# Optimization experiments

Hardware: AMD Instinct MI355X
Metric: run time of the kernel (lower is better)

Reference implementation:

```python
import jax, jax.numpy as jnp
import numpy as np

C, K, H = 256, 64, 1024


def squash(t):
    # t: [C, H]; norm = sum of squares over last dim (matches torch code)
    norm = jnp.sum(t * t, axis=-1, keepdims=True)  # [C, 1]
    scale = norm / (1.0 + norm)
    return scale * t / jnp.sqrt(norm)


def setup_inputs() -> dict:
    key = jax.random.key(0)
    k1, k2 = jax.random.split(key)
    encoder_output = jax.random.normal(k1, (C, K, H), dtype=jnp.float32)
    # nn.Linear weight [out, in]; scaled init for numerical sanity
    W = jax.random.normal(k2, (H, H), dtype=jnp.float32) * (1.0 / np.sqrt(H))
    return {"encoder_output": encoder_output, "W": W, "iter_routing": 3}


def reference(encoder_output, W, iter_routing):
    # encoder_output: [C, K, H], W: [H, H] (l_1 weight, no bias)
    # The linear projection is loop-invariant in the original; hoist it.
    x_hat = jnp.einsum('ckh,dh->ckd', encoder_output, W)  # [C, K, H]
    b = jnp.zeros(encoder_output.shape[:2], dtype=encoder_output.dtype)  # [C, K]
    c = None
    for _ in range(iter_routing):
        d = jax.nn.softmax(b, axis=-1)                       # [C, K]
        c_hat = jnp.sum(x_hat * d[..., None], axis=1)        # [C, H]
        c = squash(c_hat)                                    # [C, H]
        b = b + jnp.einsum('ckh,ch->ck', x_hat, c)           # [C, K]
    return c
```

## Files before the change

### kernel.cpp

```cpp
#include <hip/hip_runtime.h>


using f32x4  = __attribute__((ext_vector_type(4))) float;
using f32x2  = __attribute__((ext_vector_type(2))) float;
using bf16x8 = __attribute__((ext_vector_type(8))) __bf16;
using bf16x4 = __attribute__((ext_vector_type(4))) __bf16;

struct BfPair { __bf16 hi, lo; };
__device__ inline BfPair split_bf16(float x) {
    BfPair p;
    p.hi = (__bf16)x;
    p.lo = (__bf16)(x - (float)p.hi);
    return p;
}

template <int MODE>
__global__ __launch_bounds__(1024, 4) void routing_kernel(
    const float* __restrict__ enc, const float* __restrict__ y0,
    const float* __restrict__ y1, float* __restrict__ bglob,
    __bf16* __restrict__ s_hi, __bf16* __restrict__ s_lo)
{
    __shared__ float spart[16][1024];
    __shared__ float u_s[1024];
    __shared__ float b_s[64], d_s[64], red_s[16], scale_s;

    const int t = threadIdx.x, lane = t & 63, w = t >> 6;
    const int c = blockIdx.x;
    const float* E = enc + (size_t)c * 65536;

    float yv = 0.f, sv = 0.f;
    if (MODE > 0) {
        const size_t o = (size_t)c * 1024 + t;
        yv = y0[o] + y1[o];
        sv = (float)s_hi[o] + (float)s_lo[o];
    }

    f32x4 er[4][4];
    #pragma unroll
    for (int r = 0; r < 4; ++r) {
        const float* ek = E + (size_t)(w * 4 + r) * 1024 + lane * 8;
        er[r][0] = *(const f32x4*)(ek);
        er[r][1] = *(const f32x4*)(ek + 4);
        er[r][2] = *(const f32x4*)(ek + 512);
        er[r][3] = *(const f32x4*)(ek + 516);
    }
    #pragma unroll
    for (int r = 0; r < 4; ++r)
        #pragma unroll
        for (int q = 0; q < 4; ++q)
            asm volatile("" : "+v"(er[r][q]));

    if (MODE > 0) {
        u_s[t] = yv;
        float p = yv * sv;
        #pragma unroll
        for (int off = 32; off; off >>= 1) p += __shfl_xor(p, off, 64);
        if (lane == 0) red_s[w] = p;
        __syncthreads();
        if (t == 0) {
            float n = 0.f;
            #pragma unroll
            for (int i = 0; i < 16; ++i) n += red_s[i];
            scale_s = n / ((1.f + n) * sqrtf(n) + 1e-30f);
        }
        __syncthreads();
        const float scale = scale_s;
        f32x4 uf[4];
        uf[0] = *(const f32x4*)&u_s[lane * 8];
        uf[1] = *(const f32x4*)&u_s[lane * 8 + 4];
        uf[2] = *(const f32x4*)&u_s[512 + lane * 8];
        uf[3] = *(const f32x4*)&u_s[512 + lane * 8 + 4];
        #pragma unroll
        for (int r = 0; r < 4; ++r) {
            float sum = 0.f;
            #pragma unroll
            for (int q = 0; q < 4; ++q)
                #pragma unroll
                for (int j = 0; j < 4; ++j)
                    sum += er[r][q][j] * uf[q][j];
            #pragma unroll
            for (int off = 32; off; off >>= 1) sum += __shfl_xor(sum, off, 64);
            if (lane == 0) {
                const int k = w * 4 + r;
                const float bv =
                    (MODE == 2 ? bglob[c * 64 + k] : 0.f) + scale * sum;
                bglob[c * 64 + k] = bv;
                b_s[k] = bv;
            }
        }
    }
    __syncthreads();

    if (MODE == 0) {
        if (t < 64) d_s[t] = 1.f / 64.f;
    } else if (t < 64) {
        float bv = b_s[t], m = bv;
        #pragma unroll
        for (int off = 32; off; off >>= 1) m = fmaxf(m, __shfl_xor(m, off, 64));
        const float e = expf(bv - m);
        float sm = e;
        #pragma unroll
        for (int off = 32; off; off >>= 1) sm += __shfl_xor(sm, off, 64);
        d_s[t] = e / sm;
    }
    __syncthreads();

    #pragma unroll
    for (int q = 0; q < 4; ++q) {
        f32x4 p = {};
        #pragma unroll
        for (int r = 0; r < 4; ++r) {
            const float dk = d_s[w * 4 + r];
            #pragma unroll
            for (int j = 0; j < 4; ++j) p[j] += dk * er[r][q][j];
        }
        const int h = (q >> 1) * 512 + lane * 8 + (q & 1) * 4;
        *(f32x4*)&spart[w][h] = p;
    }
    __syncthreads();

    {
        float a = 0.f;
        #pragma unroll
        for (int wv = 0; wv < 16; ++wv) a += spart[wv][t];
        const BfPair p = split_bf16(a);
        s_hi[(size_t)c * 1024 + t] = p.hi;
        s_lo[(size_t)c * 1024 + t] = p.lo;
    }
}

struct QSmem {
    __bf16 a_hi[64 * 64];
    __bf16 a_lo[64 * 64];
    __bf16 b_hi[64 * 64];
    __bf16 b_lo[64 * 64];
};

__device__ __forceinline__ int swz128(int row, int colbyte) {
    return row * 128 + (colbyte ^ ((row & 7) << 4));
}

__global__ __launch_bounds__(256) void gemm_q_kernel(
    const __bf16* __restrict__ Wt_hi, const __bf16* __restrict__ Wt_lo,
    __bf16* __restrict__ Q_hi, __bf16* __restrict__ Q_lo)
{
    __shared__ QSmem sm;
    const int qb = blockIdx.x;
    const int ti = qb >> 4, tj = qb & 15;
    const int t = threadIdx.x;
    const int lane = t & 63, w = t >> 6;
    const int wr = w >> 1, wc = w & 1;
    const int sr  = t >> 2;
    const int scb = (t & 3) * 16;
    const size_t ga = (size_t)(ti * 64 + sr) * 1024 + scb / 2;
    const size_t gb = (size_t)(tj * 64 + sr) * 1024 + scb / 2;

    f32x4 acc[2][2] = {};
    for (int k0 = 0; k0 < 1024; k0 += 64) {
        if (k0) __syncthreads();
        #pragma unroll
        for (int h = 0; h < 2; ++h) {
            const int cb = scb + h * 64;
            const size_t gao = ga + h * 32 + k0;
            const size_t gbo = gb + h * 32 + k0;
            *(bf16x8*)((char*)sm.a_hi + swz128(sr, cb)) = *(const bf16x8*)(Wt_hi + gao);
            *(bf16x8*)((char*)sm.a_lo + swz128(sr, cb)) = *(const bf16x8*)(Wt_lo + gao);
            *(bf16x8*)((char*)sm.b_hi + swz128(sr, cb)) = *(const bf16x8*)(Wt_hi + gbo);
            *(bf16x8*)((char*)sm.b_lo + swz128(sr, cb)) = *(const bf16x8*)(Wt_lo + gbo);
        }
        __syncthreads();
        #pragma unroll
        for (int kk = 0; kk < 2; ++kk) {
            const int cb = kk * 64 + (lane >> 4) * 16;
            bf16x8 ah[2], al[2], bh[2], bl[2];
            #pragma unroll
            for (int mi = 0; mi < 2; ++mi) {
                const int m = wr * 32 + mi * 16 + (lane & 15);
                ah[mi] = *(const bf16x8*)((char*)sm.a_hi + swz128(m, cb));
                al[mi] = *(const bf16x8*)((char*)sm.a_lo + swz128(m, cb));
            }
            #pragma unroll
            for (int ni = 0; ni < 2; ++ni) {
                const int n = wc * 32 + ni * 16 + (lane & 15);
                bh[ni] = *(const bf16x8*)((char*)sm.b_hi + swz128(n, cb));
                bl[ni] = *(const bf16x8*)((char*)sm.b_lo + swz128(n, cb));
            }
            #pragma unroll
            for (int mi = 0; mi < 2; ++mi)
                #pragma unroll
                for (int ni = 0; ni < 2; ++ni) {
                    f32x4 a = acc[mi][ni];
                    a = __builtin_amdgcn_mfma_f32_16x16x32_bf16(ah[mi], bh[ni], a, 0, 0, 0);
                    a = __builtin_amdgcn_mfma_f32_16x16x32_bf16(ah[mi], bl[ni], a, 0, 0, 0);
                    a = __builtin_amdgcn_mfma_f32_16x16x32_bf16(al[mi], bh[ni], a, 0, 0, 0);
                    acc[mi][ni] = a;
                }
        }
    }
    const int rr = (lane >> 4) * 4, colb = lane & 15;
    #pragma unroll
    for (int mi = 0; mi < 2; ++mi)
        #pragma unroll
        for (int ni = 0; ni < 2; ++ni)
            #pragma unroll
            for (int r = 0; r < 4; ++r) {
                const BfPair p = split_bf16(acc[mi][ni][r]);
                const size_t idx =
                    (size_t)(ti * 64 + wr * 32 + mi * 16 + rr + r) * 1024 +
                    tj * 64 + wc * 32 + ni * 16 + colb;
                Q_hi[idx] = p.hi;
                Q_lo[idx] = p.lo;
            }
}

template <int CONV>
__global__ __launch_bounds__(256) void gemm_split_kernel(
    const __bf16* __restrict__ Ah, const __bf16* __restrict__ Al,
    const __bf16* __restrict__ Bh, const __bf16* __restrict__ Bl,
    float* __restrict__ C0, float* __restrict__ C1,
    const float* __restrict__ Wsrc, __bf16* __restrict__ Wd_hi,
    __bf16* __restrict__ Wd_lo)
{
    if (CONV && blockIdx.x >= 512) {
        const int b = blockIdx.x - 512;
        const size_t base = (size_t)b * 4096 + (threadIdx.x << 2);
        #pragma unroll
        for (int q = 0; q < 4; ++q) {
            const size_t idx = base + (size_t)q * 1024;
            const f32x4 v = *(const f32x4*)(Wsrc + idx);
            bf16x4 hv, lv;
            #pragma unroll
            for (int j = 0; j < 4; ++j) {
                const BfPair p = split_bf16(v[j]);
                hv[j] = p.hi;
                lv[j] = p.lo;
            }
            *(bf16x4*)(Wd_hi + idx) = hv;
            *(bf16x4*)(Wd_lo + idx) = lv;
        }
        return;
    }

    const int w = threadIdx.x >> 6;
    const int gw = blockIdx.x * 4 + w;
    const int task = gw >> 1;
    const int kh   = gw & 1;
    const int mt   = task >> 6;
    const int nt   = task & 63;
    const int lane = threadIdx.x & 63;
    const int kq   = (lane >> 4) * 8 + kh * 512;
    const size_t aoff = (size_t)(mt * 16 + (lane & 15)) * 1024 + kq;
    const size_t boff = (size_t)(nt * 16 + (lane & 15)) * 1024 + kq;

    f32x4 hh = {}, hl = {}, lh = {};
    #pragma unroll 4
    for (int k0 = 0; k0 < 512; k0 += 32) {
        bf16x8 ah = *(const bf16x8*)(Ah + aoff + k0);
        bf16x8 al = *(const bf16x8*)(Al + aoff + k0);
        bf16x8 bh = *(const bf16x8*)(Bh + boff + k0);
        bf16x8 bl = *(const bf16x8*)(Bl + boff + k0);
        hh = __builtin_amdgcn_mfma_f32_16x16x32_bf16(ah, bh, hh, 0, 0, 0);
        hl = __builtin_amdgcn_mfma_f32_16x16x32_bf16(ah, bl, hl, 0, 0, 0);
        lh = __builtin_amdgcn_mfma_f32_16x16x32_bf16(al, bh, lh, 0, 0, 0);
    }
    f32x4 acc = hh + hl + lh;
    float* Cc = kh ? C1 : C0;
    const int rr = (lane >> 4) * 4, colb = lane & 15;
    #pragma unroll
    for (int r = 0; r < 4; ++r)
        Cc[(size_t)(mt * 16 + rr + r) * 1024 + nt * 16 + colb] = acc[r];
}

__global__ __launch_bounds__(256) void squash_out_kernel(
    const float* __restrict__ chat0, const float* __restrict__ chat1,
    float* __restrict__ outp)
{
    __shared__ float wsum[4];
    const int c = blockIdx.x, t = threadIdx.x;
    const int lane = t & 63, w = t >> 6;
    const size_t o = (size_t)c * 1024 + t * 4;
    f32x4 v = *(const f32x4*)(chat0 + o) + *(const f32x4*)(chat1 + o);
    float ss = v[0]*v[0] + v[1]*v[1] + v[2]*v[2] + v[3]*v[3];
    #pragma unroll
    for (int off = 32; off; off >>= 1) ss += __shfl_xor(ss, off, 64);
    if (lane == 0) wsum[w] = ss;
    __syncthreads();
    const float norm = wsum[0] + wsum[1] + wsum[2] + wsum[3];
    const float scale = norm / ((1.f + norm) * sqrtf(norm) + 1e-30f);
    *(f32x4*)(outp + o) = v * scale;
}

__global__ __launch_bounds__(256) void convert_wt_kernel(
    const float* __restrict__ W, __bf16* __restrict__ Wt_hi,
    __bf16* __restrict__ Wt_lo)
{
    __shared__ float tile[64][65];
    const int bx = blockIdx.x, by = blockIdx.y;
    const int tx = threadIdx.x & 63, ty = threadIdx.x >> 6;
    for (int i = ty; i < 64; i += 4)
        tile[i][tx] = W[(size_t)(by * 64 + i) * 1024 + bx * 64 + tx];
    __syncthreads();
    for (int i = ty; i < 64; i += 4) {
        const size_t idx = (size_t)(bx * 64 + i) * 1024 + by * 64 + tx;
        const BfPair p = split_bf16(tile[tx][i]);
        Wt_hi[idx] = p.hi;
        Wt_lo[idx] = p.lo;
    }
}

__global__ __launch_bounds__(512) void fallback_kernel(
    const float* __restrict__ enc, const float* __restrict__ W,
    float* __restrict__ outp)
{
    __shared__ float u_s[1024], s_s[1024], c_s[1024], chat_s[1024];
    __shared__ float b_s[64], d_s[64], red_s[8];
    const int t = threadIdx.x, lane = t & 63, w = t >> 6;
    const float* erow = enc + (size_t)blockIdx.x * 65536;

    if (t < 64) b_s[t] = 0.f;
    __syncthreads();

    for (int it = 0; it < 3; ++it) {
        if (it > 0) {
            f32x4 uf[4];
            #pragma unroll
            for (int q = 0; q < 2; ++q) {
                uf[2*q]   = *(const f32x4*)&u_s[q*512 + lane*8];
                uf[2*q+1] = *(const f32x4*)&u_s[q*512 + lane*8 + 4];
            }
            for (int r = 0; r < 8; ++r) {
                const int k = w * 8 + r;
                const float* ek = erow + (size_t)k * 1024;
                float sum = 0.f;
                #pragma unroll
                for (int q = 0; q < 2; ++q) {
                    f32x4 e0 = *(const f32x4*)(ek + q*512 + lane*8);
                    f32x4 e1 = *(const f32x4*)(ek + q*512 + lane*8 + 4);
                    #pragma unroll
                    for (int j = 0; j < 4; ++j) {
                        sum += e0[j] * uf[2*q][j];
                        sum += e1[j] * uf[2*q+1][j];
                    }
                }
                #pragma unroll
                for (int off = 32; off; off >>= 1) sum += __shfl_xor(sum, off, 64);
                if (lane == 0) b_s[k] += sum;
            }
            __syncthreads();
        }
        if (t < 64) {
            float bv = b_s[t], m = bv;
            #pragma unroll
            for (int off = 32; off; off >>= 1) m = fmaxf(m, __shfl_xor(m, off, 64));
            float e = expf(bv - m), sm = e;
            #pragma unroll
            for (int off = 32; off; off >>= 1) sm += __shfl_xor(sm, off, 64);
            d_s[t] = e / sm;
        }
        __syncthreads();
        {
            const int h0 = t * 2;
            float a0 = 0.f, a1 = 0.f;
            for (int k = 0; k < 64; ++k) {
                f32x2 ev = *(const f32x2*)(erow + (size_t)k * 1024 + h0);
                a0 += d_s[k] * ev[0]; a1 += d_s[k] * ev[1];
            }
            s_s[h0] = a0; s_s[h0+1] = a1;
        }
        __syncthreads();
        {
            f32x4 sf[4];
            #pragma unroll
            for (int q = 0; q < 2; ++q) {
                sf[2*q]   = *(const f32x4*)&s_s[q*512 + lane*8];
                sf[2*q+1] = *(const f32x4*)&s_s[q*512 + lane*8 + 4];
            }
            for (int r = 0; r < 128; ++r) {
                const int d = w * 128 + r;
                const float* wr = W + (size_t)d * 1024;
                float sum = 0.f;
                #pragma unroll
                for (int q = 0; q < 2; ++q) {
                    f32x4 w0 = *(const f32x4*)(wr + q*512 + lane*8);
                    f32x4 w1 = *(const f32x4*)(wr + q*512 + lane*8 + 4);
                    #pragma unroll
                    for (int j = 0; j < 4; ++j) {
                        sum += w0[j] * sf[2*q][j];
                        sum += w1[j] * sf[2*q+1][j];
                    }
                }
                #pragma unroll
                for (int off = 32; off; off >>= 1) sum += __shfl_xor(sum, off, 64);
                if (lane == 0) chat_s[d] = sum;
            }
        }
        __syncthreads();
        {
            const int h0 = t * 2;
            float v0 = chat_s[h0], v1 = chat_s[h0+1];
            float ss = v0*v0 + v1*v1;
            #pragma unroll
            for (int off = 32; off; off >>= 1) ss += __shfl_xor(ss, off, 64);
            if (lane == 0) red_s[w] = ss;
            __syncthreads();
            float norm = 0.f;
            #pragma unroll
            for (int i = 0; i < 8; ++i) norm += red_s[i];
            const float scale = norm / ((1.f + norm) * sqrtf(norm) + 1e-30f);
            c_s[h0] = v0 * scale; c_s[h0+1] = v1 * scale;
        }
        __syncthreads();
        if (it < 2) {
            const int h0 = t * 2;
            float uu0 = 0.f, uu1 = 0.f;
            for (int d = 0; d < 1024; ++d) {
                f32x2 wv = *(const f32x2*)(W + (size_t)d * 1024 + h0);
                uu0 += c_s[d] * wv[0]; uu1 += c_s[d] * wv[1];
            }
            u_s[h0] = uu0; u_s[h0+1] = uu1;
        } else {
            const int h0 = t * 2;
            f32x2 ov; ov[0] = c_s[h0]; ov[1] = c_s[h0+1];
            *(f32x2*)(outp + (size_t)blockIdx.x * 1024 + h0) = ov;
        }
        __syncthreads();
    }
}

extern "C" void kernel_launch(void* const* d_in, const int* in_sizes, int n_in,
                              void* d_out, int out_size, void* d_ws, size_t ws_size,
                              hipStream_t stream)
{
    const float* enc = (const float*)d_in[0];
    const float* W   = (const float*)d_in[1];
    float* outp = (float*)d_out;
    (void)in_sizes; (void)n_in; (void)out_size;

    char* ws = (char*)d_ws;
    float*  b     = (float*) (ws + 0x000000);
    __bf16* s_hi  = (__bf16*)(ws + 0x080000);
    __bf16* s_lo  = (__bf16*)(ws + 0x100000);
    float*  y0    = (float*) (ws + 0x180000);
    float*  y1    = (float*) (ws + 0x280000);
    __bf16* Wx_hi = (__bf16*)(ws + 0x380000);
    __bf16* Wx_lo = (__bf16*)(ws + 0x580000);
    __bf16* Q_hi  = (__bf16*)(ws + 0x780000);
    __bf16* Q_lo  = (__bf16*)(ws + 0x980000);

    if (ws_size < 0xB80000) {
        fallback_kernel<<<256, 512, 0, stream>>>(enc, W, outp);
        return;
    }

    convert_wt_kernel<<<dim3(16, 16), 256, 0, stream>>>(W, Wx_hi, Wx_lo);

    gemm_q_kernel<<<256, 256, 0, stream>>>(Wx_hi, Wx_lo, Q_hi, Q_lo);

    routing_kernel<0><<<256, 1024, 0, stream>>>(enc, y0, y1, b, s_hi, s_lo);

    gemm_split_kernel<1><<<768, 256, 0, stream>>>(
        s_hi, s_lo, Q_hi, Q_lo, y0, y1, W, Wx_hi, Wx_lo);

    routing_kernel<1><<<256, 1024, 0, stream>>>(enc, y0, y1, b, s_hi, s_lo);

    gemm_split_kernel<0><<<512, 256, 0, stream>>>(
        s_hi, s_lo, Q_hi, Q_lo, y0, y1, nullptr, nullptr, nullptr);

    routing_kernel<2><<<256, 1024, 0, stream>>>(enc, y0, y1, b, s_hi, s_lo);

    gemm_split_kernel<0><<<512, 256, 0, stream>>>(
        s_hi, s_lo, Wx_hi, Wx_lo, y0, y1, nullptr, nullptr, nullptr);

    squash_out_kernel<<<256, 256, 0, stream>>>(y0, y1, outp);
}
```

Before: 199.2 us.

## Tile split-bf16 GEMMs through swizzled LDS and fuse W conversion into routing

```diff
diff --git a/kernel.cpp b/kernel.cpp
--- a/kernel.cpp
+++ b/kernel.cpp
@@ -14,18 +14,19 @@
     return p;
 }
 
+struct RoutSM {
+    float spart[16][1024];
+    float u_s[1024];
+    float b_s[64], d_s[64], red_s[16], scale_s;
+};
+
 template <int MODE>
-__global__ __launch_bounds__(1024, 4) void routing_kernel(
-    const float* __restrict__ enc, const float* __restrict__ y0,
+__device__ __forceinline__ void routing_body(
+    int c, const float* __restrict__ enc, const float* __restrict__ y0,
     const float* __restrict__ y1, float* __restrict__ bglob,
-    __bf16* __restrict__ s_hi, __bf16* __restrict__ s_lo)
-{
-    __shared__ float spart[16][1024];
-    __shared__ float u_s[1024];
-    __shared__ float b_s[64], d_s[64], red_s[16], scale_s;
-
+    __bf16* __restrict__ s_hi, __bf16* __restrict__ s_lo, RoutSM* sm)
+{
     const int t = threadIdx.x, lane = t & 63, w = t >> 6;
-    const int c = blockIdx.x;
     const float* E = enc + (size_t)c * 65536;
 
     float yv = 0.f, sv = 0.f;
@@ -51,25 +52,25 @@
             asm volatile("" : "+v"(er[r][q]));
 
     if (MODE > 0) {
-        u_s[t] = yv;
+        sm->u_s[t] = yv;
         float p = yv * sv;
         #pragma unroll
         for (int off = 32; off; off >>= 1) p += __shfl_xor(p, off, 64);
-        if (lane == 0) red_s[w] = p;
+        if (lane == 0) sm->red_s[w] = p;
         __syncthreads();
         if (t == 0) {
             float n = 0.f;
             #pragma unroll
-            for (int i = 0; i < 16; ++i) n += red_s[i];
-            scale_s = n / ((1.f + n) * sqrtf(n) + 1e-30f);
-        }
-        __syncthreads();
-        const float scale = scale_s;
+            for (int i = 0; i < 16; ++i) n += sm->red_s[i];
+            sm->scale_s = n / ((1.f + n) * sqrtf(n) + 1e-30f);
+        }
+        __syncthreads();
+        const float scale = sm->scale_s;
         f32x4 uf[4];
-        uf[0] = *(const f32x4*)&u_s[lane * 8];
-        uf[1] = *(const f32x4*)&u_s[lane * 8 + 4];
-        uf[2] = *(const f32x4*)&u_s[512 + lane * 8];
-        uf[3] = *(const f32x4*)&u_s[512 + lane * 8 + 4];
+        uf[0] = *(const f32x4*)&sm->u_s[lane * 8];
+        uf[1] = *(const f32x4*)&sm->u_s[lane * 8 + 4];
+        uf[2] = *(const f32x4*)&sm->u_s[512 + lane * 8];
+        uf[3] = *(const f32x4*)&sm->u_s[512 + lane * 8 + 4];
         #pragma unroll
         for (int r = 0; r < 4; ++r) {
             float sum = 0.f;
@@ -85,23 +86,23 @@
                 const float bv =
                     (MODE == 2 ? bglob[c * 64 + k] : 0.f) + scale * sum;
                 bglob[c * 64 + k] = bv;
-                b_s[k] = bv;
+                sm->b_s[k] = bv;
             }
         }
     }
     __syncthreads();
 
     if (MODE == 0) {
-        if (t < 64) d_s[t] = 1.f / 64.f;
+        if (t < 64) sm->d_s[t] = 1.f / 64.f;
     } else if (t < 64) {
-        float bv = b_s[t], m = bv;
+        float bv = sm->b_s[t], m = bv;
         #pragma unroll
         for (int off = 32; off; off >>= 1) m = fmaxf(m, __shfl_xor(m, off, 64));
         const float e = expf(bv - m);
-        float sm = e;
-        #pragma unroll
-        for (int off = 32; off; off >>= 1) sm += __shfl_xor(sm, off, 64);
-        d_s[t] = e / sm;
+        float smm = e;
+        #pragma unroll
+        for (int off = 32; off; off >>= 1) smm += __shfl_xor(smm, off, 64);
+        sm->d_s[t] = e / smm;
     }
     __syncthreads();
 
@@ -110,23 +111,57 @@
         f32x4 p = {};
         #pragma unroll
         for (int r = 0; r < 4; ++r) {
-            const float dk = d_s[w * 4 + r];
+            const float dk = sm->d_s[w * 4 + r];
             #pragma unroll
             for (int j = 0; j < 4; ++j) p[j] += dk * er[r][q][j];
         }
         const int h = (q >> 1) * 512 + lane * 8 + (q & 1) * 4;
-        *(f32x4*)&spart[w][h] = p;
+        *(f32x4*)&sm->spart[w][h] = p;
     }
     __syncthreads();
 
     {
         float a = 0.f;
         #pragma unroll
-        for (int wv = 0; wv < 16; ++wv) a += spart[wv][t];
+        for (int wv = 0; wv < 16; ++wv) a += sm->spart[wv][t];
         const BfPair p = split_bf16(a);
         s_hi[(size_t)c * 1024 + t] = p.hi;
         s_lo[(size_t)c * 1024 + t] = p.lo;
     }
+}
+
+template <int MODE, int WITH_CONV>
+__global__ __launch_bounds__(1024, 4) void routing_kernel(
+    const float* __restrict__ enc, const float* __restrict__ y0,
+    const float* __restrict__ y1, float* __restrict__ bglob,
+    __bf16* __restrict__ s_hi, __bf16* __restrict__ s_lo,
+    const float* __restrict__ W, __bf16* __restrict__ Wt_hi,
+    __bf16* __restrict__ Wt_lo)
+{
+    __shared__ union {
+        RoutSM r;
+        float tile[64][65];
+    } sm;
+
+    int c = blockIdx.x;
+    if (WITH_CONV) {
+        if (blockIdx.x < 256) {
+            const int by = blockIdx.x >> 4, bx = blockIdx.x & 15;
+            const int tx = threadIdx.x & 63, ty = threadIdx.x >> 6;
+            for (int i = ty; i < 64; i += 16)
+                sm.tile[i][tx] = W[(size_t)(by * 64 + i) * 1024 + bx * 64 + tx];
+            __syncthreads();
+            for (int i = ty; i < 64; i += 16) {
+                const size_t idx = (size_t)(bx * 64 + i) * 1024 + by * 64 + tx;
+                const BfPair p = split_bf16(sm.tile[tx][i]);
+                Wt_hi[idx] = p.hi;
+                Wt_lo[idx] = p.lo;
+            }
+            return;
+        }
+        c = blockIdx.x - 256;
+    }
+    routing_body<MODE>(c, enc, y0, y1, bglob, s_hi, s_lo, &sm.r);
 }
 
 struct QSmem {
@@ -214,15 +249,16 @@
 }
 
 template <int CONV>
-__global__ __launch_bounds__(256) void gemm_split_kernel(
+__global__ __launch_bounds__(256) void gemm_nt_kernel(
     const __bf16* __restrict__ Ah, const __bf16* __restrict__ Al,
     const __bf16* __restrict__ Bh, const __bf16* __restrict__ Bl,
     float* __restrict__ C0, float* __restrict__ C1,
     const float* __restrict__ Wsrc, __bf16* __restrict__ Wd_hi,
     __bf16* __restrict__ Wd_lo)
 {
-    if (CONV && blockIdx.x >= 512) {
-        const int b = blockIdx.x - 512;
+    __shared__ QSmem sm;
+    if (CONV && blockIdx.x >= 128) {
+        const int b = blockIdx.x - 128;
         const size_t base = (size_t)b * 4096 + (threadIdx.x << 2);
         #pragma unroll
         for (int q = 0; q < 4; ++q) {
@@ -241,34 +277,70 @@
         return;
     }
 
-    const int w = threadIdx.x >> 6;
-    const int gw = blockIdx.x * 4 + w;
-    const int task = gw >> 1;
-    const int kh   = gw & 1;
-    const int mt   = task >> 6;
-    const int nt   = task & 63;
-    const int lane = threadIdx.x & 63;
-    const int kq   = (lane >> 4) * 8 + kh * 512;
-    const size_t aoff = (size_t)(mt * 16 + (lane & 15)) * 1024 + kq;
-    const size_t boff = (size_t)(nt * 16 + (lane & 15)) * 1024 + kq;
-
-    f32x4 hh = {}, hl = {}, lh = {};
-    #pragma unroll 4
-    for (int k0 = 0; k0 < 512; k0 += 32) {
-        bf16x8 ah = *(const bf16x8*)(Ah + aoff + k0);
-        bf16x8 al = *(const bf16x8*)(Al + aoff + k0);
-        bf16x8 bh = *(const bf16x8*)(Bh + boff + k0);
-        bf16x8 bl = *(const bf16x8*)(Bl + boff + k0);
-        hh = __builtin_amdgcn_mfma_f32_16x16x32_bf16(ah, bh, hh, 0, 0, 0);
-        hl = __builtin_amdgcn_mfma_f32_16x16x32_bf16(ah, bl, hl, 0, 0, 0);
-        lh = __builtin_amdgcn_mfma_f32_16x16x32_bf16(al, bh, lh, 0, 0, 0);
-    }
-    f32x4 acc = hh + hl + lh;
+    const int kh   = blockIdx.x & 1;
+    const int task = blockIdx.x >> 1;
+    const int mt   = task >> 4;
+    const int nt   = task & 15;
+    const int t = threadIdx.x;
+    const int lane = t & 63, w = t >> 6;
+    const int wr = w >> 1, wc = w & 1;
+    const int sr  = t >> 2;
+    const int scb = (t & 3) * 16;
+    const size_t ga = (size_t)(mt * 64 + sr) * 1024 + kh * 512 + scb / 2;
+    const size_t gb = (size_t)(nt * 64 + sr) * 1024 + kh * 512 + scb / 2;
+
+    f32x4 acc[2][2] = {};
+    for (int k0 = 0; k0 < 512; k0 += 64) {
+        if (k0) __syncthreads();
+        #pragma unroll
+        for (int h = 0; h < 2; ++h) {
+            const int cb = scb + h * 64;
+            const size_t gao = ga + h * 32 + k0;
+            const size_t gbo = gb + h * 32 + k0;
+            *(bf16x8*)((char*)sm.a_hi + swz128(sr, cb)) = *(const bf16x8*)(Ah + gao);
+            *(bf16x8*)((char*)sm.a_lo + swz128(sr, cb)) = *(const bf16x8*)(Al + gao);
+            *(bf16x8*)((char*)sm.b_hi + swz128(sr, cb)) = *(const bf16x8*)(Bh + gbo);
+            *(bf16x8*)((char*)sm.b_lo + swz128(sr, cb)) = *(const bf16x8*)(Bl + gbo);
+        }
+        __syncthreads();
+        #pragma unroll
+        for (int kk = 0; kk < 2; ++kk) {
+            const int cb = kk * 64 + (lane >> 4) * 16;
+            bf16x8 ah[2], al[2], bh[2], bl[2];
+            #pragma unroll
+            for (int mi = 0; mi < 2; ++mi) {
+                const int m = wr * 32 + mi * 16 + (lane & 15);
+                ah[mi] = *(const bf16x8*)((char*)sm.a_hi + swz128(m, cb));
+                al[mi] = *(const bf16x8*)((char*)sm.a_lo + swz128(m, cb));
+            }
+            #pragma unroll
+            for (int ni = 0; ni < 2; ++ni) {
+                const int n = wc * 32 + ni * 16 + (lane & 15);
+                bh[ni] = *(const bf16x8*)((char*)sm.b_hi + swz128(n, cb));
+                bl[ni] = *(const bf16x8*)((char*)sm.b_lo + swz128(n, cb));
+            }
+            #pragma unroll
+            for (int mi = 0; mi < 2; ++mi)
+                #pragma unroll
+                for (int ni = 0; ni < 2; ++ni) {
+                    f32x4 a = acc[mi][ni];
+                    a = __builtin_amdgcn_mfma_f32_16x16x32_bf16(ah[mi], bh[ni], a, 0, 0, 0);
+                    a = __builtin_amdgcn_mfma_f32_16x16x32_bf16(ah[mi], bl[ni], a, 0, 0, 0);
+                    a = __builtin_amdgcn_mfma_f32_16x16x32_bf16(al[mi], bh[ni], a, 0, 0, 0);
+                    acc[mi][ni] = a;
+                }
+        }
+    }
     float* Cc = kh ? C1 : C0;
     const int rr = (lane >> 4) * 4, colb = lane & 15;
     #pragma unroll
-    for (int r = 0; r < 4; ++r)
-        Cc[(size_t)(mt * 16 + rr + r) * 1024 + nt * 16 + colb] = acc[r];
+    for (int mi = 0; mi < 2; ++mi)
+        #pragma unroll
+        for (int ni = 0; ni < 2; ++ni)
+            #pragma unroll
+            for (int r = 0; r < 4; ++r)
+                Cc[(size_t)(mt * 64 + wr * 32 + mi * 16 + rr + r) * 1024 +
+                   nt * 64 + wc * 32 + ni * 16 + colb] = acc[mi][ni][r];
 }
 
 __global__ __launch_bounds__(256) void squash_out_kernel(
@@ -290,24 +362,6 @@
     *(f32x4*)(outp + o) = v * scale;
 }
 
-__global__ __launch_bounds__(256) void convert_wt_kernel(
-    const float* __restrict__ W, __bf16* __restrict__ Wt_hi,
-    __bf16* __restrict__ Wt_lo)
-{
-    __shared__ float tile[64][65];
-    const int bx = blockIdx.x, by = blockIdx.y;
-    const int tx = threadIdx.x & 63, ty = threadIdx.x >> 6;
-    for (int i = ty; i < 64; i += 4)
-        tile[i][tx] = W[(size_t)(by * 64 + i) * 1024 + bx * 64 + tx];
-    __syncthreads();
-    for (int i = ty; i < 64; i += 4) {
-        const size_t idx = (size_t)(bx * 64 + i) * 1024 + by * 64 + tx;
-        const BfPair p = split_bf16(tile[tx][i]);
-        Wt_hi[idx] = p.hi;
-        Wt_lo[idx] = p.lo;
-    }
-}
-
 __global__ __launch_bounds__(512) void fallback_kernel(
     const float* __restrict__ enc, const float* __restrict__ W,
     float* __restrict__ outp)
@@ -452,23 +506,24 @@
         return;
     }
 
-    convert_wt_kernel<<<dim3(16, 16), 256, 0, stream>>>(W, Wx_hi, Wx_lo);
+    routing_kernel<0, 1><<<512, 1024, 0, stream>>>(
+        enc, y0, y1, b, s_hi, s_lo, W, Wx_hi, Wx_lo);
 
     gemm_q_kernel<<<256, 256, 0, stream>>>(Wx_hi, Wx_lo, Q_hi, Q_lo);
 
-    routing_kernel<0><<<256, 1024, 0, stream>>>(enc, y0, y1, b, s_hi, s_lo);
-
-    gemm_split_kernel<1><<<768, 256, 0, stream>>>(
+    gemm_nt_kernel<1><<<384, 256, 0, stream>>>(
         s_hi, s_lo, Q_hi, Q_lo, y0, y1, W, Wx_hi, Wx_lo);
 
-    routing_kernel<1><<<256, 1024, 0, stream>>>(enc, y0, y1, b, s_hi, s_lo);
-
-    gemm_split_kernel<0><<<512, 256, 0, stream>>>(
+    routing_kernel<1, 0><<<256, 1024, 0, stream>>>(
+        enc, y0, y1, b, s_hi, s_lo, nullptr, nullptr, nullptr);
+
+    gemm_nt_kernel<0><<<128, 256, 0, stream>>>(
         s_hi, s_lo, Q_hi, Q_lo, y0, y1, nullptr, nullptr, nullptr);
 
-    routing_kernel<2><<<256, 1024, 0, stream>>>(enc, y0, y1, b, s_hi, s_lo);
-
-    gemm_split_kernel<0><<<512, 256, 0, stream>>>(
+    routing_kernel<2, 0><<<256, 1024, 0, stream>>>(
+        enc, y0, y1, b, s_hi, s_lo, nullptr, nullptr, nullptr);
+
+    gemm_nt_kernel<0><<<128, 256, 0, stream>>>(
         s_hi, s_lo, Wx_hi, Wx_lo, y0, y1, nullptr, nullptr, nullptr);
 
     squash_out_kernel<<<256, 256, 0, stream>>>(y0, y1, outp);
```

After: 186.0 us. 1.07x faster.
